# Kernel tuning notes

Hardware: AMD Instinct MI355X
Metric: run time of the kernel (lower is better)

## Reference

```python
import jax, jax.numpy as jnp
import numpy as np
import math

BS, S, D, H = 16, 512, 1024, 16
DK = D // H
HALF = H // 2
R, GAMMA, EPS = 1.0, 0.1, 1e-6


def _alibi(n_heads, maxpos):
    # n_heads=16 is a power of 2
    start = 2.0 ** (-2.0 ** (-(math.log2(n_heads) - 3)))
    slopes = np.array([start * start ** i for i in range(n_heads)], dtype=np.float32) * -1.0
    pos = np.arange(maxpos)
    rel = np.abs(pos[None, :] - pos[:, None]).astype(np.float32)
    return jnp.asarray((slopes[:, None, None] * rel)[None])  # (1,H,maxpos,maxpos)


def setup_inputs() -> dict:
    key = jax.random.key(0)
    ks = jax.random.split(key, 6)
    sc = 1.0 / math.sqrt(D)
    x = jax.random.normal(ks[0], (BS, S, D), dtype=jnp.float32)
    Wq = jax.random.normal(ks[1], (D, D), dtype=jnp.float32) * sc
    Wk = jax.random.normal(ks[2], (D, D), dtype=jnp.float32) * sc
    Wv = jax.random.normal(ks[3], (D, D), dtype=jnp.float32) * sc
    Wo = jax.random.normal(ks[4], (D, D), dtype=jnp.float32) * sc
    bq = jnp.zeros((D,), jnp.float32)
    bk = jnp.zeros((D,), jnp.float32)
    bv = jnp.zeros((D,), jnp.float32)
    bo = jnp.zeros((D,), jnp.float32)
    alibi = _alibi(H, S)  # pre-sliced to seq_len (original slices [:,:,:S,:S])
    # src_mask for mask=0: np.triu(ones,k=0)==0 -> strictly lower triangular
    mask = jnp.tril(jnp.ones((S, S), dtype=bool), k=-1)[None, None]
    return {"x": x, "Wq": Wq, "bq": bq, "Wk": Wk, "bk": bk, "Wv": Wv,
            "bv": bv, "Wo": Wo, "bo": bo, "alibi": alibi, "mask": mask}


def _map_psi(x, r):
    x_y = jax.nn.sigmoid(x[..., -1])           # (b,h,s)
    return x[..., :-1] * x_y[..., None] * r, x_y * r


def _penumbral(q, k, r=R, gamma=GAMMA, eps=EPS):
    q_x, q_y = _map_psi(q, r)
    k_x, k_y = _map_psi(k, r)
    q_y = q_y[..., :, None]                    # (b,h,s,1)
    k_y = k_y[..., None, :]                    # (b,h,1,s)
    x_q_y = jnp.sqrt(r ** 2 - q_y ** 2 + eps)
    x_k_y = jnp.sqrt(r ** 2 - k_y ** 2 + eps)
    # euclidean cdist over last dim (d_k-1)
    qn = jnp.sum(q_x ** 2, axis=-1)[..., :, None]
    kn = jnp.sum(k_x ** 2, axis=-1)[..., None, :]
    d2 = qn + kn - 2.0 * jnp.einsum('bhqd,bhkd->bhqk', q_x, k_x)
    pd = jnp.sqrt(jnp.maximum(d2, 0.0) + 1e-12)
    lca = jnp.maximum(jnp.maximum(q_y ** 2, k_y ** 2),
                      r ** 2 - ((x_q_y + x_k_y - pd) / 2.0) ** 2)
    lca_out = ((pd ** 2 + k_y ** 2 - q_y ** 2) / (2.0 * pd + eps)) ** 2 + q_y ** 2
    exists = (pd <= x_q_y) | ((pd - x_q_y) ** 2 + k_y ** 2 <= r ** 2)
    return -gamma * jnp.where(exists, lca, lca_out)


def _masked_softmax_zeropad(scores, mask):
    scores = jnp.where(mask, scores, -1e32)
    p = jax.nn.softmax(scores, axis=-1)
    return p.at[:, :, 0, :].set(0.0)  # zero_pad=True (mask==0 branch)


def reference(x, Wq, bq, Wk, bk, Wv, bv, Wo, bo, alibi, mask):
    bs, s, d = x.shape
    q = (x @ Wq.T + bq).reshape(bs, s, H, DK).transpose(0, 2, 1, 3)
    k = (x @ Wk.T + bk).reshape(bs, s, H, DK).transpose(0, 2, 1, 3)
    v = (x @ Wv.T + bv).reshape(bs, s, H, DK).transpose(0, 2, 1, 3)
    inv = 1.0 / math.sqrt(DK)
    # first half heads: standard dot-product attention + alibi
    sc1 = jnp.einsum('bhqd,bhkd->bhqk', q[:, :HALF], k[:, :HALF]) * inv
    sc1 = sc1 + alibi[:, :HALF, :s, :s]
    p1 = _masked_softmax_zeropad(sc1, mask)
    o1 = jnp.einsum('bhqk,bhkd->bhqd', p1, v[:, :HALF])
    # second half heads: penumbral hyperbolic score + alibi
    sc2 = _penumbral(q[:, HALF:], k[:, HALF:]) * inv
    sc2 = sc2 + alibi[:, HALF:, :s, :s]
    p2 = _masked_softmax_zeropad(sc2, mask)
    o2 = jnp.einsum('bhqk,bhkd->bhqd', p2, v[:, HALF:])
    out = jnp.concatenate([o1, o2], axis=1)  # (b,H,s,dk)
    out = out.transpose(0, 2, 1, 3).reshape(bs, s, d)
    return out @ Wo.T + bo
```

## Files before the change

### kernel.cpp

```cpp
#include <hip/hip_runtime.h>
#include <math.h>

#define BS 16
#define S 512
#define D 1024
#define H 16
#define DK 64
#define HALF 8

typedef __attribute__((ext_vector_type(8))) short short8v;
typedef __attribute__((ext_vector_type(4))) float f32x4;
typedef unsigned short ushort_t;

#define L2E 1.4426950408889634f
#define SC_STD (0.125f * L2E)
#define SC_PEN (-0.0125f * L2E)

__device__ __forceinline__ ushort_t f2bf(float f) {
  union { float f; unsigned u; } v; v.f = f;
  unsigned r = v.u + 0x7fffu + ((v.u >> 16) & 1u);
  return (ushort_t)(r >> 16);
}
__device__ __forceinline__ unsigned packbf(float a, float b) {
  return (unsigned)f2bf(a) | ((unsigned)f2bf(b) << 16);
}
__device__ __forceinline__ float bf2f(ushort_t u) {
  union { unsigned u; float f; } v; v.u = ((unsigned)u) << 16;
  return v.f;
}
__device__ __forceinline__ unsigned cvtpk(float lo, float hi) {
  unsigned r;
  asm("v_cvt_pk_bf16_f32 %0, %1, %2" : "=v"(r) : "v"(lo), "v"(hi));
  return r;
}

__device__ __forceinline__ void gload16(const void* g, void* l) {
  __builtin_amdgcn_global_load_lds(
      (const __attribute__((address_space(1))) unsigned int*)g,
      (__attribute__((address_space(3))) unsigned int*)l, 16, 0, 0);
}

#define WAIT_VM(n) asm volatile("s_waitcnt vmcnt(" #n ")" ::: "memory")

__global__ __launch_bounds__(256) void cvt_fused(
    const float* __restrict__ x, const float* __restrict__ Wq,
    const float* __restrict__ Wk, const float* __restrict__ Wv,
    const float* __restrict__ Wo, ushort_t* __restrict__ dst) {
  const int bid = blockIdx.x;
  const float* src;
  int si;
  if (bid < 4096) {
    src = x; si = bid * 256 + threadIdx.x;
  } else {
    const int k = bid - 4096;
    const int w = k >> 9;
    src = (w == 0) ? Wq : (w == 1) ? Wk : (w == 2) ? Wv : Wo;
    si = (k & 511) * 256 + threadIdx.x;
  }
  const int di = bid * 256 + threadIdx.x;
  const float4 a = *(const float4*)(src + (size_t)si * 8);
  const float4 b = *(const float4*)(src + (size_t)si * 8 + 4);
  union { short8v v; unsigned u[4]; } t;
  t.u[0] = packbf(a.x, a.y);
  t.u[1] = packbf(a.z, a.w);
  t.u[2] = packbf(b.x, b.y);
  t.u[3] = packbf(b.z, b.w);
  *(short8v*)(dst + (size_t)di * 8) = t.v;
}

__global__ __launch_bounds__(256) void gemm_qkv(
    const ushort_t* __restrict__ A, const ushort_t* __restrict__ Wcat,
    const float* __restrict__ bq, const float* __restrict__ bk,
    const float* __restrict__ bv, ushort_t* __restrict__ QK,
    ushort_t* __restrict__ Vt, float4* __restrict__ QPn,
    float4* __restrict__ KPn) {
  const int id = blockIdx.x;
  const int xcd = id & 7, r0 = id >> 3;
  const int bn = xcd * 3 + (r0 % 3);
  const int bm = r0 / 3;
  const int tid = threadIdx.x;
  const int lane = tid & 63, wid = tid >> 6;
  const int wr = wid >> 1, wc = wid & 1;
  const int lq = lane & 15, g = lane >> 4;
  const int mat = bn >> 3;

  __shared__ __align__(16) ushort_t sA[2][128 * 64];
  __shared__ __align__(16) ushort_t sB[2][128 * 64];

  f32x4 acc[4][4];
#pragma unroll
  for (int i = 0; i < 4; i++)
#pragma unroll
    for (int j = 0; j < 4; j++) acc[i][j] = (f32x4){0.f, 0.f, 0.f, 0.f};

  auto stage = [&](int buf, int k0) {
#pragma unroll
    for (int is = 0; is < 4; ++is) {
      const int gi = is * 256 + tid;
      const int row = gi >> 3, slot = gi & 7;
      const int sslot = slot ^ (row & 7);
      gload16(A + (size_t)(bm * 128 + row) * 1024 + k0 + sslot * 8,
              &sA[buf][(is * 256 + wid * 64) * 8]);
      gload16(Wcat + (size_t)(bn * 128 + row) * 1024 + k0 + sslot * 8,
              &sB[buf][(is * 256 + wid * 64) * 8]);
    }
  };

  stage(0, 0);
  WAIT_VM(0);
  __builtin_amdgcn_s_barrier();
  for (int t = 0; t < 16; ++t) {
    if (t < 15) {
      stage((t + 1) & 1, (t + 1) * 64);
      WAIT_VM(8);
    } else {
      WAIT_VM(0);
    }
    __builtin_amdgcn_s_barrier();
    __builtin_amdgcn_sched_barrier(0);
    const int buf = t & 1;
#pragma unroll
    for (int ks = 0; ks < 2; ++ks) {
      short8v af[4], bf[4];
#pragma unroll
      for (int i = 0; i < 4; ++i) {
        const int arow = wr * 64 + i * 16 + lq;
        af[i] = *(const short8v*)&sA[buf][arow * 64 + (((ks * 4 + g) ^ (arow & 7)) * 8)];
        const int brow = wc * 64 + i * 16 + lq;
        bf[i] = *(const short8v*)&sB[buf][brow * 64 + (((ks * 4 + g) ^ (brow & 7)) * 8)];
      }
#pragma unroll
      for (int i = 0; i < 4; ++i)
#pragma unroll
        for (int j = 0; j < 4; ++j)
          acc[i][j] =
              __builtin_amdgcn_mfma_f32_16x16x32_bf16(af[i], bf[j], acc[i][j], 0, 0, 0);
    }
    __builtin_amdgcn_s_barrier();
  }

  const float* bias = (mat == 0) ? bq : (mat == 1) ? bk : bv;
  const size_t NQKV = (size_t)BS * H * S * DK;

  if (mat < 2) {
    const int headq = (bn & 7) * 2 + wc;
    const bool penq = (headq >= HALF);
    float4* Pn = (mat == 0) ? QPn : KPn;
    ushort_t* Cbase = QK + (size_t)mat * NQKV;
#pragma unroll
    for (int i = 0; i < 4; ++i) {
      const int mb = bm * 128 + wr * 64 + i * 16 + g * 4;
      float cc[4][4];
#pragma unroll
      for (int j = 0; j < 4; ++j) {
        const int n = ((bn & 7) * 128) + wc * 64 + j * 16 + lq;
        const float bvv = bias[n];
#pragma unroll
        for (int r = 0; r < 4; ++r) cc[j][r] = acc[i][j][r] + bvv;
      }
      float yv[4] = {0.f, 0.f, 0.f, 0.f};
      if (penq) {
#pragma unroll
        for (int r = 0; r < 4; ++r) {
          const float last = __shfl(cc[3][r], (lane & 48) + 15, 64);
          yv[r] = 1.0f / (1.0f + __expf(-last));
        }
#pragma unroll
        for (int j = 0; j < 4; ++j)
#pragma unroll
          for (int r = 0; r < 4; ++r) cc[j][r] *= yv[r];
        if (lq == 15) {
#pragma unroll
          for (int r = 0; r < 4; ++r) cc[3][r] = yv[r];
        }
      }
      unsigned pk[4][2];
#pragma unroll
      for (int j = 0; j < 4; ++j) {
        pk[j][0] = cvtpk(cc[j][0], cc[j][1]);
        pk[j][1] = cvtpk(cc[j][2], cc[j][3]);
      }
#pragma unroll
      for (int j = 0; j < 4; ++j) {
        const int n = ((bn & 7) * 128) + wc * 64 + j * 16 + lq;
        ushort_t* base = Cbase +
                         ((((size_t)(mb >> 9) * H + (n >> 6)) * S + (mb & 511)) * DK) +
                         (n & 63);
        base[0] = (ushort_t)pk[j][0];
        base[DK] = (ushort_t)(pk[j][0] >> 16);
        base[2 * DK] = (ushort_t)pk[j][1];
        base[3 * DK] = (ushort_t)(pk[j][1] >> 16);
      }
      if (penq) {
        float sq[4] = {0.f, 0.f, 0.f, 0.f};
#pragma unroll
        for (int j = 0; j < 4; ++j)
#pragma unroll
          for (int r = 0; r < 4; ++r) {
            const unsigned h16 =
                (r & 1) ? (pk[j][r >> 1] >> 16) : (pk[j][r >> 1] & 0xffffu);
            float xr = bf2f((ushort_t)h16);
            if (j == 3 && lq == 15) xr = 0.f;
            sq[r] += xr * xr;
          }
#pragma unroll
        for (int mk = 1; mk <= 8; mk <<= 1)
#pragma unroll
          for (int r = 0; r < 4; ++r) sq[r] += __shfl_xor(sq[r], mk, 64);
        if (lq == 0) {
          const int hh = headq - HALF;
#pragma unroll
          for (int r = 0; r < 4; ++r) {
            const int m = mb + r;
            const int bb = m >> 9, ss = m & 511;
            Pn[((size_t)bb * HALF + hh) * S + ss] = make_float4(
                sq[r], yv[r] * yv[r], sqrtf(1.0f - yv[r] * yv[r] + 1e-6f), 0.f);
          }
        }
      }
    }
  } else {
#pragma unroll
    for (int j = 0; j < 4; ++j) {
      const int n = ((bn & 7) * 128) + wc * 64 + j * 16 + lq;
      const float bvv = bias[n];
#pragma unroll
      for (int i = 0; i < 4; ++i) {
        const int mb = bm * 128 + wr * 64 + i * 16 + g * 4;
        const int bb = mb >> 9, s0 = mb & 511;
        uint2 u;
        u.x = cvtpk(acc[i][j][0] + bvv, acc[i][j][1] + bvv);
        u.y = cvtpk(acc[i][j][2] + bvv, acc[i][j][3] + bvv);
        *(uint2*)(Vt + (((size_t)bb * H + (n >> 6)) * DK + (n & 63)) * S + s0) = u;
      }
    }
  }
}

__global__ __launch_bounds__(256) void gemm_out(
    const ushort_t* __restrict__ A, const ushort_t* __restrict__ B,
    const float* __restrict__ bias, float* __restrict__ C) {
  const int id = blockIdx.x;
  const int bn = id & 7, bm = id >> 3;
  const int tid = threadIdx.x;
  const int lane = tid & 63, wid = tid >> 6;
  const int wr = wid >> 1, wc = wid & 1;
  const int lq = lane & 15, g = lane >> 4;

  __shared__ __align__(16) ushort_t sA[2][128 * 64];
  __shared__ __align__(16) ushort_t sB[2][128 * 64];

  f32x4 acc[4][4];
#pragma unroll
  for (int i = 0; i < 4; i++)
#pragma unroll
    for (int j = 0; j < 4; j++) acc[i][j] = (f32x4){0.f, 0.f, 0.f, 0.f};

  auto stage = [&](int buf, int k0) {
#pragma unroll
    for (int is = 0; is < 4; ++is) {
      const int gi = is * 256 + tid;
      const int row = gi >> 3, slot = gi & 7;
      const int sslot = slot ^ (row & 7);
      gload16(A + (size_t)(bm * 128 + row) * 1024 + k0 + sslot * 8,
              &sA[buf][(is * 256 + wid * 64) * 8]);
      gload16(B + (size_t)(bn * 128 + row) * 1024 + k0 + sslot * 8,
              &sB[buf][(is * 256 + wid * 64) * 8]);
    }
  };

  stage(0, 0);
  WAIT_VM(0);
  __builtin_amdgcn_s_barrier();
  for (int t = 0; t < 16; ++t) {
    if (t < 15) {
      stage((t + 1) & 1, (t + 1) * 64);
      WAIT_VM(8);
    } else {
      WAIT_VM(0);
    }
    __builtin_amdgcn_s_barrier();
    __builtin_amdgcn_sched_barrier(0);
    const int buf = t & 1;
#pragma unroll
    for (int ks = 0; ks < 2; ++ks) {
      short8v af[4], bf[4];
#pragma unroll
      for (int i = 0; i < 4; ++i) {
        const int arow = wr * 64 + i * 16 + lq;
        af[i] = *(const short8v*)&sA[buf][arow * 64 + (((ks * 4 + g) ^ (arow & 7)) * 8)];
        const int brow = wc * 64 + i * 16 + lq;
        bf[i] = *(const short8v*)&sB[buf][brow * 64 + (((ks * 4 + g) ^ (brow & 7)) * 8)];
      }
#pragma unroll
      for (int i = 0; i < 4; ++i)
#pragma unroll
        for (int j = 0; j < 4; ++j)
          acc[i][j] =
              __builtin_amdgcn_mfma_f32_16x16x32_bf16(af[i], bf[j], acc[i][j], 0, 0, 0);
    }
    __builtin_amdgcn_s_barrier();
  }

#pragma unroll
  for (int j = 0; j < 4; ++j) {
    const int n = bn * 128 + wc * 64 + j * 16 + lq;
    const float bvv = bias[n];
#pragma unroll
    for (int i = 0; i < 4; ++i) {
      const int mb = bm * 128 + wr * 64 + i * 16 + g * 4;
#pragma unroll
      for (int r = 0; r < 4; ++r)
        C[(size_t)(mb + r) * 1024 + n] = acc[i][j][r] + bvv;
    }
  }
}

template <bool MASK>
__device__ __forceinline__ void attn_tile(
    const char* sKb, const char* sVb, const float4* sPn, const short8v* qf,
    float qn, float qy2, float xqy, bool pen, float slopeL, int qg, int kt0,
    int lq, int g, f32x4* o, float& m, float& lacc) {
  float p[4][4];
  float tmax = -1e30f;
#pragma unroll
  for (int t4 = 0; t4 < 4; ++t4) {
    f32x4 acc = (f32x4){0.f, 0.f, 0.f, 0.f};
    const int row = t4 * 16 + lq;
#pragma unroll
    for (int c = 0; c < 2; ++c) {
      const short8v ka =
          *(const short8v*)(sKb + row * 128 + (((c * 4 + g) ^ (row & 7)) * 16));
      acc = __builtin_amdgcn_mfma_f32_16x16x32_bf16(ka, qf[c], acc, 0, 0, 0);
    }
#pragma unroll
    for (int r = 0; r < 4; ++r) {
      const int kg = kt0 + t4 * 16 + g * 4 + r;
      const float abL = slopeL * (float)(qg - kg);
      float s;
      if (!pen) {
        s = acc[r] * SC_STD + abL;
      } else {
        const float4 kp = sPn[t4 * 16 + g * 4 + r];
        const float kn = kp.x, ky2 = kp.y, xky = kp.z;
        const float d2 = qn + kn - 2.0f * acc[r];
        const float tt = fmaxf(d2, 0.0f) + 1e-12f;
        const float rs = rsqrtf(tt);
        const float pd = tt * rs;
        const float tmp = (xqy + xky - pd) * 0.5f;
        const float lca = fmaxf(fmaxf(qy2, ky2), 1.0f - tmp * tmp);
        const float num = (d2 + ky2 - qy2) * (0.5f * rs);
        const float lout = num * num + qy2;
        const float dxy = pd - xqy;
        const bool ex = (pd <= xqy) || (dxy * dxy + ky2 <= 1.0f);
        s = (ex ? lca : lout) * SC_PEN + abL;
      }
      if (MASK && kg >= qg) s = -1e30f;
      p[t4][r] = s;
      tmax = fmaxf(tmax, s);
    }
  }
  tmax = fmaxf(tmax, __shfl_xor(tmax, 16, 64));
  tmax = fmaxf(tmax, __shfl_xor(tmax, 32, 64));
  const float mnew = fmaxf(m, tmax);
  if (__any(mnew > m)) {
    const float fsc = exp2f(m - mnew);
#pragma unroll
    for (int dt = 0; dt < 4; ++dt) o[dt] *= fsc;
    lacc *= fsc;
    m = mnew;
  }
  float ls = 0.f;
#pragma unroll
  for (int t4 = 0; t4 < 4; ++t4)
#pragma unroll
    for (int r = 0; r < 4; ++r) {
      float pv = exp2f(p[t4][r] - m);
      if (MASK && p[t4][r] < -1e29f) pv = 0.f;
      p[t4][r] = pv;
      ls += pv;
    }
  ls += __shfl_xor(ls, 16, 64);
  ls += __shfl_xor(ls, 32, 64);
  lacc += ls;

  unsigned pk0[4], pk1[4];
#pragma unroll
  for (int t4 = 0; t4 < 4; ++t4) {
    pk0[t4] = cvtpk(p[t4][0], p[t4][1]);
    pk1[t4] = cvtpk(p[t4][2], p[t4][3]);
  }
  const int s0 = lq | (((g * 2) & 3) << 4);
  const int s1 = lq | (((g * 2 + 1) & 3) << 4);
  const bool hi = (g >= 2);
#pragma unroll
  for (int c = 0; c < 2; ++c) {
    const unsigned a0 = (unsigned)__shfl((int)pk0[2 * c], s0, 64);
    const unsigned b0 = (unsigned)__shfl((int)pk0[2 * c + 1], s0, 64);
    const unsigned a1 = (unsigned)__shfl((int)pk1[2 * c], s0, 64);
    const unsigned b1 = (unsigned)__shfl((int)pk1[2 * c + 1], s0, 64);
    const unsigned a2 = (unsigned)__shfl((int)pk0[2 * c], s1, 64);
    const unsigned b2 = (unsigned)__shfl((int)pk0[2 * c + 1], s1, 64);
    const unsigned a3 = (unsigned)__shfl((int)pk1[2 * c], s1, 64);
    const unsigned b3 = (unsigned)__shfl((int)pk1[2 * c + 1], s1, 64);
    union { short8v v; unsigned u[4]; } pb;
    pb.u[0] = hi ? b0 : a0;
    pb.u[1] = hi ? b1 : a1;
    pb.u[2] = hi ? b2 : a2;
    pb.u[3] = hi ? b3 : a3;
#pragma unroll
    for (int dt = 0; dt < 4; ++dt) {
      const int vr = dt * 16 + lq;
      const short8v va =
          *(const short8v*)(sVb + vr * 128 + (((c * 4 + g) ^ (vr & 7)) * 16));
      o[dt] = __builtin_amdgcn_mfma_f32_16x16x32_bf16(va, pb.v, o[dt], 0, 0, 0);
    }
  }
}

__global__ __launch_bounds__(256, 4) void attn_mfma(
    const ushort_t* __restrict__ Qf, const ushort_t* __restrict__ Kf,
    const ushort_t* __restrict__ Vt, const float4* __restrict__ QPn,
    const float4* __restrict__ KPn, ushort_t* __restrict__ O) {
  const int dsp = blockIdx.x;
  const int xcd = dsp & 7, idx = dsp >> 3;
  const int bh = xcd * 32 + (idx & 31);
  const int qb = 7 - (idx >> 5);
  const int b = bh >> 4, h = bh & 15;
  const int tid = threadIdx.x, lane = tid & 63, wid = tid >> 6;
  const int lq = lane & 15, g = lane >> 4;
  const bool pen = (h >= HALF);
  const float slopeL = -exp2f(-0.5f * (float)(h + 1)) * L2E;
  const size_t hoff = ((size_t)b * H + h) * S * DK;
  const ushort_t* Vslab = Vt + hoff;
  const size_t bhh = (size_t)b * HALF + (h & (HALF - 1));

  __shared__ __align__(16) char sK[2][8192];
  __shared__ __align__(16) char sV[2][8192];
  __shared__ __align__(16) float4 sPen[2][64];

  const int qg = qb * 64 + wid * 16 + lq;

  short8v qf[2];
  {
    const ushort_t* qr = Qf + hoff + (size_t)qg * DK;
    qf[0] = *(const short8v*)(qr + g * 8);
    qf[1] = *(const short8v*)(qr + 32 + g * 8);
    if (pen && g == 3) qf[1][7] = 0;
  }
  float qn = 0, qy2 = 0, xqy = 0;
  if (pen) {
    const float4 a = QPn[bhh * S + qg];
    qn = a.x; qy2 = a.y; xqy = a.z;
  }

  const int r8 = lane >> 3;
  const int sl = ((lane & 7) ^ r8) * 8;

  const bool extra = pen && (wid == 0);
  auto stage = [&](int buf, int kt) {
#pragma unroll
    for (int i = 0; i < 2; ++i) {
      const int row = wid * 16 + i * 8 + r8;
      gload16(Kf + hoff + (size_t)(kt * 64 + row) * DK + sl,
              &sK[buf][(wid * 2 + i) * 1024]);
      gload16(Vslab + (size_t)row * S + kt * 64 + sl,
              &sV[buf][(wid * 2 + i) * 1024]);
    }
    if (extra)
      gload16(&KPn[bhh * S + kt * 64 + lane], &sPen[buf][0]);
  };

  f32x4 o[4];
#pragma unroll
  for (int dt = 0; dt < 4; ++dt) o[dt] = (f32x4){0.f, 0.f, 0.f, 0.f};
  float m = -1e30f, l = 0.f;

  stage(0, qb);
  WAIT_VM(0);
  __builtin_amdgcn_s_barrier();
  int cur = 0;
  for (int kt = qb; kt >= 0; --kt) {
    if (kt > 0) {
      stage(cur ^ 1, kt - 1);
      if (extra) { WAIT_VM(5); } else { WAIT_VM(4); }
    } else {
      WAIT_VM(0);
    }
    __builtin_amdgcn_s_barrier();
    __builtin_amdgcn_sched_barrier(0);
    if (kt == qb)
      attn_tile<true>(sK[cur], sV[cur], sPen[cur], qf, qn, qy2, xqy, pen,
                      slopeL, qg, kt * 64, lq, g, o, m, l);
    else
      attn_tile<false>(sK[cur], sV[cur], sPen[cur], qf, qn, qy2, xqy, pen,
                       slopeL, qg, kt * 64, lq, g, o, m, l);
    __builtin_amdgcn_s_barrier();
    cur ^= 1;
  }

  const float invl = (qg == 0) ? 0.f : 1.0f / l;
  ushort_t* orow = O + ((size_t)b * S + qg) * D + h * DK;
#pragma unroll
  for (int dt = 0; dt < 4; ++dt) {
    uint2 u;
    u.x = cvtpk(o[dt][0] * invl, o[dt][1] * invl);
    u.y = cvtpk(o[dt][2] * invl, o[dt][3] * invl);
    *(uint2*)(orow + dt * 16 + g * 4) = u;
  }
}

extern "C" void kernel_launch(void* const* d_in, const int* in_sizes, int n_in,
                              void* d_out, int out_size, void* d_ws,
                              size_t ws_size, hipStream_t stream) {
  (void)in_sizes; (void)n_in; (void)out_size; (void)ws_size;
  const float* x  = (const float*)d_in[0];
  const float* Wq = (const float*)d_in[1];
  const float* bq = (const float*)d_in[2];
  const float* Wk = (const float*)d_in[3];
  const float* bk = (const float*)d_in[4];
  const float* Wv = (const float*)d_in[5];
  const float* bv = (const float*)d_in[6];
  const float* Wo = (const float*)d_in[7];
  const float* bo = (const float*)d_in[8];
  float* out = (float*)d_out;

  const size_t NQKV = (size_t)BS * H * S * DK;
  const size_t NW = (size_t)D * D;
  ushort_t* ws  = (ushort_t*)d_ws;
  ushort_t* Qb  = ws;
  ushort_t* Kbb = Qb + NQKV;
  ushort_t* Vtb = Kbb + NQKV;
  ushort_t* Ob  = Vtb + NQKV;
  ushort_t* xb  = Ob + NQKV;
  ushort_t* Wqb = xb + NQKV;
  ushort_t* Wkb = Wqb + NW;
  ushort_t* Wvb = Wkb + NW;
  ushort_t* Wob = Wvb + NW;
  float4* QPn = (float4*)(Wob + NW);
  float4* KPn = QPn + (size_t)BS * HALF * S;

  cvt_fused<<<dim3(4096 + 4 * 512), 256, 0, stream>>>(x, Wq, Wk, Wv, Wo, xb);
  gemm_qkv<<<dim3(1536), 256, 0, stream>>>(xb, Wqb, bq, bk, bv, Qb, Vtb, QPn,
                                           KPn);
  attn_mfma<<<dim3(2048), 256, 0, stream>>>(Qb, Kbb, Vtb, QPn, KPn, Ob);
  gemm_out<<<dim3(512), 256, 0, stream>>>(Ob, Wob, bo, out);
}
```

Baseline: 149.9 us.

## Use 8 waves per block in QKV and output GEMMs

Both projection GEMM kernels now run 512 threads per 128x128 tile instead of 256. Each wave owns a 32x64 sub-tile, and staging and waits are adjusted to two loads per thread. The aim is more waves to hide latency and fewer accumulator registers per wave. In exchange, B fragments are re-read from LDS by more waves and barrier overhead per block grows.

```diff
diff --git a/kernel.cpp b/kernel.cpp
--- a/kernel.cpp
+++ b/kernel.cpp
@@ -68,7 +68,7 @@
   *(short8v*)(dst + (size_t)di * 8) = t.v;
 }
 
-__global__ __launch_bounds__(256) void gemm_qkv(
+__global__ __launch_bounds__(512) void gemm_qkv(
     const ushort_t* __restrict__ A, const ushort_t* __restrict__ Wcat,
     const float* __restrict__ bq, const float* __restrict__ bk,
     const float* __restrict__ bv, ushort_t* __restrict__ QK,
@@ -87,22 +87,22 @@
   __shared__ __align__(16) ushort_t sA[2][128 * 64];
   __shared__ __align__(16) ushort_t sB[2][128 * 64];
 
-  f32x4 acc[4][4];
-#pragma unroll
-  for (int i = 0; i < 4; i++)
+  f32x4 acc[2][4];
+#pragma unroll
+  for (int i = 0; i < 2; i++)
 #pragma unroll
     for (int j = 0; j < 4; j++) acc[i][j] = (f32x4){0.f, 0.f, 0.f, 0.f};
 
   auto stage = [&](int buf, int k0) {
 #pragma unroll
-    for (int is = 0; is < 4; ++is) {
-      const int gi = is * 256 + tid;
+    for (int ld = 0; ld < 2; ++ld) {
+      const int gi = ld * 512 + tid;
       const int row = gi >> 3, slot = gi & 7;
       const int sslot = slot ^ (row & 7);
       gload16(A + (size_t)(bm * 128 + row) * 1024 + k0 + sslot * 8,
-              &sA[buf][(is * 256 + wid * 64) * 8]);
+              &sA[buf][(size_t)gi * 8]);
       gload16(Wcat + (size_t)(bn * 128 + row) * 1024 + k0 + sslot * 8,
-              &sB[buf][(is * 256 + wid * 64) * 8]);
+              &sB[buf][(size_t)gi * 8]);
     }
   };
 
@@ -112,7 +112,7 @@
   for (int t = 0; t < 16; ++t) {
     if (t < 15) {
       stage((t + 1) & 1, (t + 1) * 64);
-      WAIT_VM(8);
+      WAIT_VM(4);
     } else {
       WAIT_VM(0);
     }
@@ -121,16 +121,19 @@
     const int buf = t & 1;
 #pragma unroll
     for (int ks = 0; ks < 2; ++ks) {
-      short8v af[4], bf[4];
-#pragma unroll
-      for (int i = 0; i < 4; ++i) {
-        const int arow = wr * 64 + i * 16 + lq;
+      short8v af[2], bf[4];
+#pragma unroll
+      for (int i = 0; i < 2; ++i) {
+        const int arow = wr * 32 + i * 16 + lq;
         af[i] = *(const short8v*)&sA[buf][arow * 64 + (((ks * 4 + g) ^ (arow & 7)) * 8)];
-        const int brow = wc * 64 + i * 16 + lq;
-        bf[i] = *(const short8v*)&sB[buf][brow * 64 + (((ks * 4 + g) ^ (brow & 7)) * 8)];
-      }
-#pragma unroll
-      for (int i = 0; i < 4; ++i)
+      }
+#pragma unroll
+      for (int j = 0; j < 4; ++j) {
+        const int brow = wc * 64 + j * 16 + lq;
+        bf[j] = *(const short8v*)&sB[buf][brow * 64 + (((ks * 4 + g) ^ (brow & 7)) * 8)];
+      }
+#pragma unroll
+      for (int i = 0; i < 2; ++i)
 #pragma unroll
         for (int j = 0; j < 4; ++j)
           acc[i][j] =
@@ -148,8 +151,8 @@
     float4* Pn = (mat == 0) ? QPn : KPn;
     ushort_t* Cbase = QK + (size_t)mat * NQKV;
 #pragma unroll
-    for (int i = 0; i < 4; ++i) {
-      const int mb = bm * 128 + wr * 64 + i * 16 + g * 4;
+    for (int i = 0; i < 2; ++i) {
+      const int mb = bm * 128 + wr * 32 + i * 16 + g * 4;
       float cc[4][4];
 #pragma unroll
       for (int j = 0; j < 4; ++j) {
@@ -225,8 +228,8 @@
       const int n = ((bn & 7) * 128) + wc * 64 + j * 16 + lq;
       const float bvv = bias[n];
 #pragma unroll
-      for (int i = 0; i < 4; ++i) {
-        const int mb = bm * 128 + wr * 64 + i * 16 + g * 4;
+      for (int i = 0; i < 2; ++i) {
+        const int mb = bm * 128 + wr * 32 + i * 16 + g * 4;
         const int bb = mb >> 9, s0 = mb & 511;
         uint2 u;
         u.x = cvtpk(acc[i][j][0] + bvv, acc[i][j][1] + bvv);
@@ -237,7 +240,7 @@
   }
 }
 
-__global__ __launch_bounds__(256) void gemm_out(
+__global__ __launch_bounds__(512) void gemm_out(
     const ushort_t* __restrict__ A, const ushort_t* __restrict__ B,
     const float* __restrict__ bias, float* __restrict__ C) {
   const int id = blockIdx.x;
@@ -250,22 +253,22 @@
   __shared__ __align__(16) ushort_t sA[2][128 * 64];
   __shared__ __align__(16) ushort_t sB[2][128 * 64];
 
-  f32x4 acc[4][4];
-#pragma unroll
-  for (int i = 0; i < 4; i++)
+  f32x4 acc[2][4];
+#pragma unroll
+  for (int i = 0; i < 2; i++)
 #pragma unroll
     for (int j = 0; j < 4; j++) acc[i][j] = (f32x4){0.f, 0.f, 0.f, 0.f};
 
   auto stage = [&](int buf, int k0) {
 #pragma unroll
-    for (int is = 0; is < 4; ++is) {
-      const int gi = is * 256 + tid;
+    for (int ld = 0; ld < 2; ++ld) {
+      const int gi = ld * 512 + tid;
       const int row = gi >> 3, slot = gi & 7;
       const int sslot = slot ^ (row & 7);
       gload16(A + (size_t)(bm * 128 + row) * 1024 + k0 + sslot * 8,
-              &sA[buf][(is * 256 + wid * 64) * 8]);
+              &sA[buf][(size_t)gi * 8]);
       gload16(B + (size_t)(bn * 128 + row) * 1024 + k0 + sslot * 8,
-              &sB[buf][(is * 256 + wid * 64) * 8]);
+              &sB[buf][(size_t)gi * 8]);
     }
   };
 
@@ -275,7 +278,7 @@
   for (int t = 0; t < 16; ++t) {
     if (t < 15) {
       stage((t + 1) & 1, (t + 1) * 64);
-      WAIT_VM(8);
+      WAIT_VM(4);
     } else {
       WAIT_VM(0);
     }
@@ -284,16 +287,19 @@
     const int buf = t & 1;
 #pragma unroll
     for (int ks = 0; ks < 2; ++ks) {
-      short8v af[4], bf[4];
-#pragma unroll
-      for (int i = 0; i < 4; ++i) {
-        const int arow = wr * 64 + i * 16 + lq;
+      short8v af[2], bf[4];
+#pragma unroll
+      for (int i = 0; i < 2; ++i) {
+        const int arow = wr * 32 + i * 16 + lq;
         af[i] = *(const short8v*)&sA[buf][arow * 64 + (((ks * 4 + g) ^ (arow & 7)) * 8)];
-        const int brow = wc * 64 + i * 16 + lq;
-        bf[i] = *(const short8v*)&sB[buf][brow * 64 + (((ks * 4 + g) ^ (brow & 7)) * 8)];
-      }
-#pragma unroll
-      for (int i = 0; i < 4; ++i)
+      }
+#pragma unroll
+      for (int j = 0; j < 4; ++j) {
+        const int brow = wc * 64 + j * 16 + lq;
+        bf[j] = *(const short8v*)&sB[buf][brow * 64 + (((ks * 4 + g) ^ (brow & 7)) * 8)];
+      }
+#pragma unroll
+      for (int i = 0; i < 2; ++i)
 #pragma unroll
         for (int j = 0; j < 4; ++j)
           acc[i][j] =
@@ -307,8 +313,8 @@
     const int n = bn * 128 + wc * 64 + j * 16 + lq;
     const float bvv = bias[n];
 #pragma unroll
-    for (int i = 0; i < 4; ++i) {
-      const int mb = bm * 128 + wr * 64 + i * 16 + g * 4;
+    for (int i = 0; i < 2; ++i) {
+      const int mb = bm * 128 + wr * 32 + i * 16 + g * 4;
 #pragma unroll
       for (int r = 0; r < 4; ++r)
         C[(size_t)(mb + r) * 1024 + n] = acc[i][j][r] + bvv;
@@ -541,8 +547,8 @@
   float4* KPn = QPn + (size_t)BS * HALF * S;
 
   cvt_fused<<<dim3(4096 + 4 * 512), 256, 0, stream>>>(x, Wq, Wk, Wv, Wo, xb);
-  gemm_qkv<<<dim3(1536), 256, 0, stream>>>(xb, Wqb, bq, bk, bv, Qb, Vtb, QPn,
+  gemm_qkv<<<dim3(1536), 512, 0, stream>>>(xb, Wqb, bq, bk, bv, Qb, Vtb, QPn,
                                            KPn);
   attn_mfma<<<dim3(2048), 256, 0, stream>>>(Qb, Kbb, Vtb, QPn, KPn, Ob);
-  gemm_out<<<dim3(512), 256, 0, stream>>>(Ob, Wob, bo, out);
-}
+  gemm_out<<<dim3(512), 512, 0, stream>>>(Ob, Wob, bo, out);
+}
```

Measured after the change: 147.3 us, median of 2. About the same (-1.8%).
